# Kernel optimization log

Measured on AMD Instinct MI355X. Metric: run time of the kernel, lower is better.

Reference implementation:

```python
import jax, jax.numpy as jnp
import numpy as np
from functools import partial

N_USERS = 30000
N_ENTITIES = 70000
N = N_USERS + N_ENTITIES
D = 64
N_EDGES = 1_600_000
EPS = 1e-12


def setup_inputs() -> dict:
    key = jax.random.key(0)
    ks = jax.random.split(key, 10)
    s = 1.0 / np.sqrt(D)  # xavier-like scale for weights
    return {
        "user_tab": jax.random.normal(ks[0], (N_USERS, D), jnp.float32) * 0.1,
        "entity_tab": jax.random.normal(ks[1], (N_ENTITIES, D), jnp.float32) * 0.1,
        "A_vals": jax.random.uniform(ks[2], (N_EDGES,), jnp.float32) / 16.0,  # ~row-normalized
        "W1_1": jax.random.normal(ks[3], (D, D), jnp.float32) * s,
        "b1_1": jnp.zeros((D,), jnp.float32),
        "W2_1": jax.random.normal(ks[4], (D, D), jnp.float32) * s,
        "b2_1": jnp.zeros((D,), jnp.float32),
        "W1_2": jax.random.normal(ks[5], (D, 32), jnp.float32) * s,
        "b1_2": jnp.zeros((32,), jnp.float32),
        "W2_2": jax.random.normal(ks[6], (D, 32), jnp.float32) * s,
        "b2_2": jnp.zeros((32,), jnp.float32),
        "A_rows": jax.random.randint(ks[7], (N_EDGES,), 0, N, jnp.int64 if jax.config.jax_enable_x64 else jnp.int32),
        "A_cols": jax.random.randint(ks[8], (N_EDGES,), 0, N, jnp.int64 if jax.config.jax_enable_x64 else jnp.int32),
    }


def _spmm(rows, cols, vals, x):
    # sparse A (COO) @ dense x : gather tail embeddings, scale, scatter-add to rows
    msgs = x[cols] * vals[:, None]            # [E, d]
    return jax.ops.segment_sum(msgs, rows, num_segments=N)


def _l2norm(x):
    n = jnp.sqrt(jnp.sum(x * x, axis=1, keepdims=True))
    return x / jnp.maximum(n, EPS)


def _bi_layer(ego, side, W1, b1, W2, b2):
    sum_e = jax.nn.leaky_relu((ego + side) @ W1 + b1)  # slope 0.01 = torch default
    bi_e = jax.nn.leaky_relu((ego * side) @ W2 + b2)
    return _l2norm(sum_e + bi_e)  # dropout p=0 (eval)


def reference(user_tab, entity_tab, A_vals, W1_1, b1_1, W2_1, b2_1,
              W1_2, b1_2, W2_2, b2_2, A_rows, A_cols):
    ego = jnp.concatenate([user_tab, entity_tab], axis=0)  # [N, 64]
    all_embed = [ego]
    # layer 1: 64 -> 64
    side = _spmm(A_rows, A_cols, A_vals, ego)
    ego = _bi_layer(ego, side, W1_1, b1_1, W2_1, b2_1)
    all_embed.append(ego)
    # layer 2: 64 -> 32
    side = _spmm(A_rows, A_cols, A_vals, ego)
    ego = _bi_layer(ego, side, W1_2, b1_2, W2_2, b2_2)
    all_embed.append(ego)
    return jnp.concatenate(all_embed, axis=1)  # [N, 160]; split [n_users, n_entities] downstream
```

## Files before the change

### kernel.cpp

```cpp
#include <hip/hip_runtime.h>
#include <hip/hip_bf16.h>
#include <string.h>

#define N_USERS 30000
#define N_NODES 100000
#define DIM 64
#define N_EDGES 1600000
#define ROWS_PER_BUCK 256
#define NB ((N_NODES + ROWS_PER_BUCK - 1) / ROWS_PER_BUCK)
#define NGRP (NB * 64)
#define CHUNK 4096
#define NBLK_B ((N_EDGES + CHUNK - 1) / CHUNK)
#define BUCK_SLACK 2048
#define E_ALLOC (N_EDGES + NB * BUCK_SLACK)
#define STAGE_CAP 5120
#define GCAP 64

typedef __hip_bfloat16 bf16;
typedef __attribute__((ext_vector_type(8))) short short8;
typedef __attribute__((ext_vector_type(4))) float floatx4;

__device__ __forceinline__ float b2f(bf16 v) { return __bfloat162float(v); }
__device__ __forceinline__ bf16 f2b(float v) { return __float2bfloat16(v); }
__device__ __forceinline__ unsigned short fbits(float v) {
    bf16 b = f2b(v); unsigned short u; memcpy(&u, &b, 2); return u;
}
__device__ __forceinline__ float ubf(unsigned u) {
    return __uint_as_float(u << 16);
}

__device__ __forceinline__ float ld(const void* p, int i, int f32) {
    return f32 ? ((const float*)p)[i] : b2f(((const bf16*)p)[i]);
}
__device__ __forceinline__ void st(void* p, int i, float v, int f32) {
    if (f32) ((float*)p)[i] = v; else ((bf16*)p)[i] = f2b(v);
}
__device__ __forceinline__ unsigned short wbits(const void* p, int i, int f32) {
    return f32 ? fbits(((const float*)p)[i]) : ((const unsigned short*)p)[i];
}

__global__ void k_detect(const void* user, const void* ent, const void* vals,
                         const void* W, int* flags, int* bsize) {
    int t = threadIdx.x;
    for (int i = t; i < NB; i += 128) bsize[i] = 0;
    const void* ps[4] = { user, ent, vals, W };
    int k = t >> 5, i = t & 31;
    float v = ((const float*)ps[k])[i];
    int ok = (v == v && fabsf(v) <= 1e4f) ? 1 : 0;
    ok += __shfl_xor(ok, 1, 64);
    ok += __shfl_xor(ok, 2, 64);
    ok += __shfl_xor(ok, 4, 64);
    ok += __shfl_xor(ok, 8, 64);
    ok += __shfl_xor(ok, 16, 64);
    if ((t & 31) == 0) flags[k] = (ok >= 16) ? 1 : 0;
}

__global__ __launch_bounds__(256) void k_prepw(
    const void* W1_1, const void* b1_1, const void* W2_1, const void* b2_1,
    const void* W1_2, const void* b1_2, const void* W2_2, const void* b2_2,
    short8* wf1, float2* wsb1, short8* wf2, float* wsb2,
    const int* flags) {
    int t = threadIdx.x;
    int w = t >> 6, quad = (t >> 4) & 3, sub = t & 15;
    int fw = flags[3];
    short8 f0, f1, f2, f3;
#pragma unroll
    for (int j = 0; j < 8; ++j) {
        int k0 = quad * 8 + j, n = w * 16 + sub;
        f0[j] = (short)wbits(W1_1, k0 * 64 + n, fw);
        f1[j] = (short)wbits(W1_1, (k0 + 32) * 64 + n, fw);
        f2[j] = (short)wbits(W2_1, k0 * 64 + n, fw);
        f3[j] = (short)wbits(W2_1, (k0 + 32) * 64 + n, fw);
    }
    short8* p = wf1 + ((w * 4 + quad) * 16 + sub) * 4;
    p[0] = f0; p[1] = f1; p[2] = f2; p[3] = f3;
    if (quad == 0)
        wsb1[w * 16 + sub] = make_float2(ld(b1_1, w * 16 + sub, fw),
                                         ld(b2_1, w * 16 + sub, fw));
    int path = w >> 1, nbase = (w & 1) * 16;
    const void* W = path ? W2_2 : W1_2;
    const void* bb = path ? b2_2 : b1_2;
    short8 g0, g1;
#pragma unroll
    for (int j = 0; j < 8; ++j) {
        int k0 = quad * 8 + j, n = nbase + sub;
        g0[j] = (short)wbits(W, k0 * 32 + n, fw);
        g1[j] = (short)wbits(W, (k0 + 32) * 32 + n, fw);
    }
    short8* q = wf2 + ((w * 4 + quad) * 16 + sub) * 2;
    q[0] = g0; q[1] = g1;
    if (quad == 0) wsb2[w * 16 + sub] = ld(bb, nbase + sub, fw);
}

__global__ __launch_bounds__(256) void k_hista(const int* __restrict__ rows,
                                               int* __restrict__ cnt_table,
                                               int* __restrict__ bsize) {
    __shared__ int h[NB];
    int t = threadIdx.x, blk = blockIdx.x;
    for (int b = t; b < NB; b += 256) h[b] = 0;
    __syncthreads();
    int base = blk * CHUNK + t * 4;
#pragma unroll
    for (int it = 0; it < 4; ++it) {
        int e = base + it * 1024;
        if (e < N_EDGES) {
            int4 r = *(const int4*)&rows[e];
            atomicAdd(&h[r.x >> 8], 1);
            atomicAdd(&h[r.y >> 8], 1);
            atomicAdd(&h[r.z >> 8], 1);
            atomicAdd(&h[r.w >> 8], 1);
        }
    }
    __syncthreads();
    for (int b = t; b < NB; b += 256) {
        int v = h[b];
        cnt_table[blk * NB + b] = v;
        if (v) atomicAdd(&bsize[b], v);
    }
}

__global__ __launch_bounds__(512) void k_bscan(const int* __restrict__ bsize,
                                               int* __restrict__ bbase) {
    __shared__ int lds[512];
    int t = threadIdx.x;
    int v = (t < NB) ? (((bsize[t] + 3) & ~3) + BUCK_SLACK) : 0;
    lds[t] = v;
    __syncthreads();
    for (int off = 1; off < 512; off <<= 1) {
        int u = (t >= off) ? lds[t - off] : 0;
        __syncthreads();
        lds[t] += u;
        __syncthreads();
    }
    if (t <= NB) bbase[t] = (t == 0) ? 0 : lds[t - 1];
}

__global__ __launch_bounds__(512) void k_bscan2(int* __restrict__ cnt_table,
                                                const int* __restrict__ bbase) {
    __shared__ int lds[512];
    int t = threadIdx.x, b = blockIdx.x;
    int v = (t < NBLK_B) ? cnt_table[t * NB + b] : 0;
    lds[t] = v;
    __syncthreads();
    for (int off = 1; off < 512; off <<= 1) {
        int u = (t >= off) ? lds[t - off] : 0;
        __syncthreads();
        lds[t] += u;
        __syncthreads();
    }
    if (t < NBLK_B) cnt_table[t * NB + b] = bbase[b] + lds[t] - v;
}

__global__ __launch_bounds__(256) void k_bscatter2(
    const int* __restrict__ rows, const int* __restrict__ cols,
    const void* __restrict__ vals, const int* __restrict__ cnt_table,
    int2* __restrict__ bpack, const int* __restrict__ flags) {
    __shared__ int cur[NB];
    int t = threadIdx.x, blk = blockIdx.x;
    int fv = flags[2];
    for (int b = t; b < NB; b += 256) cur[b] = cnt_table[blk * NB + b];
    __syncthreads();
    int base = blk * CHUNK + t * 4;
#pragma unroll
    for (int it = 0; it < 4; ++it) {
        int e = base + it * 1024;
        if (e < N_EDGES) {
            int4 r = *(const int4*)&rows[e];
            int4 c = *(const int4*)&cols[e];
            float v0, v1, v2, v3;
            if (fv) {
                float4 vv = *(const float4*)((const float*)vals + e);
                v0 = vv.x; v1 = vv.y; v2 = vv.z; v3 = vv.w;
            } else {
                const bf16* bp = (const bf16*)vals + e;
                v0 = b2f(bp[0]); v1 = b2f(bp[1]); v2 = b2f(bp[2]); v3 = b2f(bp[3]);
            }
            int p0 = atomicAdd(&cur[r.x >> 8], 1);
            int p1 = atomicAdd(&cur[r.y >> 8], 1);
            int p2 = atomicAdd(&cur[r.z >> 8], 1);
            int p3 = atomicAdd(&cur[r.w >> 8], 1);
            bpack[p0] = make_int2(c.x | ((r.x & 255) << 17), __float_as_int(v0));
            bpack[p1] = make_int2(c.y | ((r.y & 255) << 17), __float_as_int(v1));
            bpack[p2] = make_int2(c.z | ((r.z & 255) << 17), __float_as_int(v2));
            bpack[p3] = make_int2(c.w | ((r.w & 255) << 17), __float_as_int(v3));
        }
    }
}

__global__ __launch_bounds__(256) void k_place2(
    const int* __restrict__ bsize, const int* __restrict__ bbase,
    const int2* __restrict__ bpack, int2* __restrict__ epack,
    int* __restrict__ grp_start, int* __restrict__ grp_len,
    int* __restrict__ perm) {
    __shared__ __align__(16) int2 stage[STAGE_CAP];
    __shared__ int rcnt[ROWS_PER_BUCK];
    __shared__ int skey[ROWS_PER_BUCK];
    __shared__ int scn[ROWS_PER_BUCK];
    __shared__ int sbr[ROWS_PER_BUCK];
    __shared__ int cur[ROWS_PER_BUCK];
    int t = threadIdx.x, b = blockIdx.x;
    int n = bsize[b];
    int gstart = bbase[b];
    rcnt[t] = 0;
    __syncthreads();
    for (int i = t; i < n; i += 256) {
        int2 p = bpack[gstart + i];
        if (i < STAGE_CAP) stage[i] = p;
        atomicAdd(&rcnt[(p.x >> 17) & 255], 1);
    }
    __syncthreads();
    int c = rcnt[t];
    int cp = (c + 3) & ~3;
    int key = (cp << 8) | t;
    __syncthreads();
    rcnt[t] = key;
    __syncthreads();
    int rank = 0;
    for (int u = 0; u < 256; ++u) rank += (rcnt[u] < key) ? 1 : 0;
    skey[rank] = key;
    __syncthreads();
    int gq = skey[t | 3] >> 8;
    scn[t] = gq;
    __syncthreads();
    for (int off = 1; off < 256; off <<= 1) {
        int u = (t >= off) ? scn[t - off] : 0;
        __syncthreads();
        scn[t] += u;
        __syncthreads();
    }
    sbr[t] = gstart + scn[t] - gq;
    __syncthreads();
    cur[t] = sbr[rank];
    int rowp = skey[t] & 255;
    int gid = b * 64 + (t >> 2);
    perm[gid * 4 + (t & 3)] = b * 256 + rowp;
    if ((t & 3) == 0) {
        grp_start[gid] = sbr[t];
        grp_len[gid] = skey[t | 3] >> 8;
    }
    __syncthreads();
    for (int i = t; i < n; i += 256) {
        int2 p = (i < STAGE_CAP) ? stage[i] : bpack[gstart + i];
        int r = (p.x >> 17) & 255;
        int pos = atomicAdd(&cur[r], 1);
        epack[pos] = make_int2((p.x & 0x1FFFF) << 7, p.y);
    }
    __syncthreads();
    int pend = sbr[rank] + (skey[rank | 3] >> 8);
    for (int pos = cur[t]; pos < pend; ++pos) epack[pos] = make_int2(0, 0);
}

__global__ void k_init(const void* __restrict__ user, const void* __restrict__ ent,
                       void* __restrict__ out, bf16* __restrict__ xb0,
                       const int* __restrict__ flags) {
    int i = blockIdx.x * blockDim.x + threadIdx.x;
    if (i >= N_NODES * DIM) return;
    int fo = flags[0], fe = flags[1];
    int n = i >> 6, d = i & 63;
    float v = (n < N_USERS) ? ld(user, i, fo) : ld(ent, i - N_USERS * DIM, fe);
    st(out, n * 160 + d, v, fo);
    xb0[i] = f2b(v);
}

#define G8_LOAD(r) \
    int b##r = (r * emx + ei) >> 1; \
    int4 qa##r = lq4[b##r], qb##r = lq4[b##r + 1]; \
    int4 qc##r = lq4[b##r + 2], qd##r = lq4[b##r + 3];

#define G8_ISSUE(r) \
    unsigned g##r##0 = *(const unsigned short*)(xbp + (unsigned)qa##r.x); \
    unsigned g##r##1 = *(const unsigned short*)(xbp + (unsigned)qa##r.z); \
    unsigned g##r##2 = *(const unsigned short*)(xbp + (unsigned)qb##r.x); \
    unsigned g##r##3 = *(const unsigned short*)(xbp + (unsigned)qb##r.z); \
    unsigned g##r##4 = *(const unsigned short*)(xbp + (unsigned)qc##r.x); \
    unsigned g##r##5 = *(const unsigned short*)(xbp + (unsigned)qc##r.z); \
    unsigned g##r##6 = *(const unsigned short*)(xbp + (unsigned)qd##r.x); \
    unsigned g##r##7 = *(const unsigned short*)(xbp + (unsigned)qd##r.z);

#define G8_FMA(r) \
    ea##r += __int_as_float(qa##r.y) * ubf(g##r##0); \
    ea##r += __int_as_float(qa##r.w) * ubf(g##r##1); \
    ea##r += __int_as_float(qb##r.y) * ubf(g##r##2); \
    ea##r += __int_as_float(qb##r.w) * ubf(g##r##3); \
    ea##r += __int_as_float(qc##r.y) * ubf(g##r##4); \
    ea##r += __int_as_float(qc##r.w) * ubf(g##r##5); \
    ea##r += __int_as_float(qd##r.y) * ubf(g##r##6); \
    ea##r += __int_as_float(qd##r.w) * ubf(g##r##7);

#define G4_LOAD(r) \
    int tb##r = (r * emx + ei) >> 1; \
    int4 ua##r = lq4[tb##r], ub##r = lq4[tb##r + 1];

#define G4_ISSUE(r) \
    unsigned h##r##0 = *(const unsigned short*)(xbp + (unsigned)ua##r.x); \
    unsigned h##r##1 = *(const unsigned short*)(xbp + (unsigned)ua##r.z); \
    unsigned h##r##2 = *(const unsigned short*)(xbp + (unsigned)ub##r.x); \
    unsigned h##r##3 = *(const unsigned short*)(xbp + (unsigned)ub##r.z);

#define G4_FMA(r) \
    ea##r += __int_as_float(ua##r.y) * ubf(h##r##0); \
    ea##r += __int_as_float(ua##r.w) * ubf(h##r##1); \
    ea##r += __int_as_float(ub##r.y) * ubf(h##r##2); \
    ea##r += __int_as_float(ub##r.w) * ubf(h##r##3);

#define FB_ROW_DECL(r) \
    int ej##r = (rs0 + r * emx) >> 1; \
    int4 eA##r = ep4[ej##r]; \
    int4 eB##r = ep4[ej##r + 1];

#define FB_ISSUE(r) \
    unsigned eg##r##0 = *(const unsigned short*)(xbp + (unsigned)eA##r.x); \
    unsigned eg##r##1 = *(const unsigned short*)(xbp + (unsigned)eA##r.z); \
    unsigned eg##r##2 = *(const unsigned short*)(xbp + (unsigned)eB##r.x); \
    unsigned eg##r##3 = *(const unsigned short*)(xbp + (unsigned)eB##r.z);

#define FB_ADV(r) \
    int4 nA##r = ep4[ej##r + 2]; \
    int4 nB##r = ep4[ej##r + 3]; \
    ej##r += 2;

#define FB_FMA(r) \
    ea##r += __int_as_float(eA##r.y) * ubf(eg##r##0); \
    ea##r += __int_as_float(eA##r.w) * ubf(eg##r##1); \
    ea##r += __int_as_float(eB##r.y) * ubf(eg##r##2); \
    ea##r += __int_as_float(eB##r.w) * ubf(eg##r##3); \
    eA##r = nA##r; eB##r = nB##r;

#define GATHER_BODY \
    float ea0 = 0.f, ea1 = 0.f, ea2 = 0.f, ea3 = 0.f; \
    if (emx <= GCAP) { \
        { \
            const int2* eps = (const int2*)epack + rs0; \
            int tot = emx << 2; \
            for (int i = lane; i < tot; i += 64) lq[i] = eps[i]; \
        } \
        int ei = 0; \
        for (; ei + 8 <= emx; ei += 8) { \
            G8_LOAD(0) G8_LOAD(1) G8_LOAD(2) G8_LOAD(3) \
            G8_ISSUE(0) G8_ISSUE(1) G8_ISSUE(2) G8_ISSUE(3) \
            G8_FMA(0) G8_FMA(1) G8_FMA(2) G8_FMA(3) \
        } \
        if (ei < emx) { \
            G4_LOAD(0) G4_LOAD(1) G4_LOAD(2) G4_LOAD(3) \
            G4_ISSUE(0) G4_ISSUE(1) G4_ISSUE(2) G4_ISSUE(3) \
            G4_FMA(0) G4_FMA(1) G4_FMA(2) G4_FMA(3) \
        } \
    } else { \
        const int4* ep4 = (const int4*)epack; \
        FB_ROW_DECL(0) FB_ROW_DECL(1) FB_ROW_DECL(2) FB_ROW_DECL(3) \
        for (int ei = 0; ei < emx; ei += 4) { \
            FB_ISSUE(0) FB_ISSUE(1) FB_ISSUE(2) FB_ISSUE(3) \
            FB_ADV(0) FB_ADV(1) FB_ADV(2) FB_ADV(3) \
            FB_FMA(0) FB_FMA(1) FB_FMA(2) FB_FMA(3) \
        } \
    }

__global__ __launch_bounds__(256) void k_layer1(
    const short8* __restrict__ wf1, const float2* __restrict__ wsb1,
    void* __restrict__ out, const int* __restrict__ grp_start,
    const int* __restrict__ grp_len, const int* __restrict__ perm,
    const int2* __restrict__ epack, const bf16* __restrict__ xt,
    bf16* __restrict__ xn, const int* __restrict__ flags) {
    __shared__ __align__(16) int2 lq_lds[4][4 * GCAP];
    __shared__ __align__(16) unsigned short hp_lds[16][72];
    __shared__ __align__(16) unsigned short hm_lds[16][72];
    __shared__ __align__(16) float ssq_lds[16][4];
    int t = threadIdx.x, lane = t & 63, w = t >> 6;
    int sub = lane & 15, quad = lane >> 4;
    int fo = flags[0];
    int gid = blockIdx.x * 4 + w;
    const char* xbp = (const char*)xt + (lane << 1);

    int rs0 = __builtin_amdgcn_readfirstlane(grp_start[gid]);
    int emx = __builtin_amdgcn_readfirstlane(grp_len[gid]);
    int4 pn = *(const int4*)&perm[gid * 4];
    int2* lq = lq_lds[w];
    const int4* lq4 = (const int4*)lq;
    GATHER_BODY
    {
        float s[4] = { ea0, ea1, ea2, ea3 };
        int nd[4] = { pn.x, pn.y, pn.z, pn.w };
#pragma unroll
        for (int r = 0; r < 4; ++r) {
            int node = (nd[r] < N_NODES) ? nd[r] : 0;
            float h = ld(out, node * 160 + lane, fo);
            hp_lds[w * 4 + r][lane] = fbits(h + s[r]);
            hm_lds[w * 4 + r][lane] = fbits(h * s[r]);
        }
    }
    __syncthreads();

    short8 Ap0 = *(const short8*)((const char*)hp_lds + sub * 144 + quad * 16);
    short8 Ap1 = *(const short8*)((const char*)hp_lds + sub * 144 + 64 + quad * 16);
    short8 Am0 = *(const short8*)((const char*)hm_lds + sub * 144 + quad * 16);
    short8 Am1 = *(const short8*)((const char*)hm_lds + sub * 144 + 64 + quad * 16);

    const short8* wfp = wf1 + ((w * 4 + quad) * 16 + sub) * 4;
    short8 Bw10 = wfp[0], Bw11 = wfp[1], Bw20 = wfp[2], Bw21 = wfp[3];
    float2 bb12 = wsb1[w * 16 + sub];
    float bias1 = bb12.x, bias2 = bb12.y;
    int wbase = w * 16;

    floatx4 c1; c1[0] = bias1; c1[1] = bias1; c1[2] = bias1; c1[3] = bias1;
    floatx4 c2; c2[0] = bias2; c2[1] = bias2; c2[2] = bias2; c2[3] = bias2;
    c1 = __builtin_amdgcn_mfma_f32_16x16x32_bf16(Ap0, Bw10, c1, 0, 0, 0);
    c1 = __builtin_amdgcn_mfma_f32_16x16x32_bf16(Ap1, Bw11, c1, 0, 0, 0);
    c2 = __builtin_amdgcn_mfma_f32_16x16x32_bf16(Am0, Bw20, c2, 0, 0, 0);
    c2 = __builtin_amdgcn_mfma_f32_16x16x32_bf16(Am1, Bw21, c2, 0, 0, 0);

    float v[4], sp[4];
#pragma unroll
    for (int r = 0; r < 4; ++r) {
        float s1 = c1[r], s2 = c2[r];
        s1 = s1 > 0.f ? s1 : 0.01f * s1;
        s2 = s2 > 0.f ? s2 : 0.01f * s2;
        v[r] = s1 + s2;
        float sq = v[r] * v[r];
        sq += __shfl_xor(sq, 1, 64);
        sq += __shfl_xor(sq, 2, 64);
        sq += __shfl_xor(sq, 4, 64);
        sq += __shfl_xor(sq, 8, 64);
        sp[r] = sq;
    }
    if (sub == 0) {
#pragma unroll
        for (int r = 0; r < 4; ++r) ssq_lds[quad * 4 + r][w] = sp[r];
    }
    __syncthreads();
    const int* pblk = perm + blockIdx.x * 16;
#pragma unroll
    for (int r = 0; r < 4; ++r) {
        int row = quad * 4 + r;
        floatx4 ps = *(const floatx4*)&ssq_lds[row][0];
        float ss = ps[0] + ps[1] + ps[2] + ps[3];
        float o = v[r] * (1.0f / fmaxf(sqrtf(ss), 1e-12f));
        int n = pblk[row];
        if (n < N_NODES) {
            st(out, n * 160 + 64 + wbase + sub, o, fo);
            xn[n * 64 + wbase + sub] = f2b(o);
        }
    }
}

__global__ __launch_bounds__(256) void k_layer2(
    const short8* __restrict__ wf2, const float* __restrict__ wsb2,
    void* __restrict__ out, const int* __restrict__ grp_start,
    const int* __restrict__ grp_len, const int* __restrict__ perm,
    const int2* __restrict__ epack, const bf16* __restrict__ xt,
    const int* __restrict__ flags) {
    __shared__ __align__(16) int2 lq_lds[4][4 * GCAP];
    __shared__ __align__(16) unsigned short hp_lds[16][72];
    __shared__ __align__(16) unsigned short hm_lds[16][72];
    __shared__ __align__(16) float bi_lds[16][32];
    __shared__ __align__(16) float ssq_lds[16][2];
    int t = threadIdx.x, lane = t & 63, w = t >> 6;
    int sub = lane & 15, quad = lane >> 4;
    int fo = flags[0];
    int gid = blockIdx.x * 4 + w;
    const char* xbp = (const char*)xt + (lane << 1);

    int rs0 = __builtin_amdgcn_readfirstlane(grp_start[gid]);
    int emx = __builtin_amdgcn_readfirstlane(grp_len[gid]);
    int4 pn = *(const int4*)&perm[gid * 4];
    int2* lq = lq_lds[w];
    const int4* lq4 = (const int4*)lq;
    GATHER_BODY
    {
        float s[4] = { ea0, ea1, ea2, ea3 };
        int nd[4] = { pn.x, pn.y, pn.z, pn.w };
#pragma unroll
        for (int r = 0; r < 4; ++r) {
            int node = (nd[r] < N_NODES) ? nd[r] : 0;
            float h = ld(out, node * 160 + 64 + lane, fo);
            hp_lds[w * 4 + r][lane] = fbits(h + s[r]);
            hm_lds[w * 4 + r][lane] = fbits(h * s[r]);
        }
    }
    __syncthreads();

    int path = w >> 1;
    int nbase = (w & 1) * 16;
    const unsigned short(*hl)[72] = path ? hm_lds : hp_lds;
    short8 Af0 = *(const short8*)((const char*)hl + sub * 144 + quad * 16);
    short8 Af1 = *(const short8*)((const char*)hl + sub * 144 + 64 + quad * 16);

    const short8* wfp = wf2 + ((w * 4 + quad) * 16 + sub) * 2;
    short8 Bf0 = wfp[0], Bf1 = wfp[1];
    float bias = wsb2[w * 16 + sub];

    floatx4 c; c[0] = bias; c[1] = bias; c[2] = bias; c[3] = bias;
    c = __builtin_amdgcn_mfma_f32_16x16x32_bf16(Af0, Bf0, c, 0, 0, 0);
    c = __builtin_amdgcn_mfma_f32_16x16x32_bf16(Af1, Bf1, c, 0, 0, 0);

    float T[4];
#pragma unroll
    for (int r = 0; r < 4; ++r) {
        float x = c[r];
        T[r] = x > 0.f ? x : 0.01f * x;
        if (path == 1) bi_lds[quad * 4 + r][nbase + sub] = T[r];
    }
    __syncthreads();

    float v[4], sp[4];
#pragma unroll
    for (int r = 0; r < 4; ++r) {
        v[r] = T[r] + bi_lds[quad * 4 + r][nbase + sub];
        float sq = v[r] * v[r];
        sq += __shfl_xor(sq, 1, 64);
        sq += __shfl_xor(sq, 2, 64);
        sq += __shfl_xor(sq, 4, 64);
        sq += __shfl_xor(sq, 8, 64);
        sp[r] = sq;
    }
    if (path == 0 && sub == 0) {
#pragma unroll
        for (int r = 0; r < 4; ++r) ssq_lds[quad * 4 + r][w & 1] = sp[r];
    }
    __syncthreads();
    if (path == 0) {
        const int* pblk = perm + blockIdx.x * 16;
#pragma unroll
        for (int r = 0; r < 4; ++r) {
            int row = quad * 4 + r;
            float ss = ssq_lds[row][0] + ssq_lds[row][1];
            float o = v[r] * (1.0f / fmaxf(sqrtf(ss), 1e-12f));
            int n = pblk[row];
            if (n < N_NODES) st(out, n * 160 + 128 + nbase + sub, o, fo);
        }
    }
}

extern "C" void kernel_launch(void* const* d_in, const int* in_sizes, int n_in,
                              void* d_out, int out_size, void* d_ws, size_t ws_size,
                              hipStream_t stream) {
    const void* user = d_in[0];
    const void* ent  = d_in[1];
    const void* vals = d_in[2];
    const void* W1_1 = d_in[3];
    const void* b1_1 = d_in[4];
    const void* W2_1 = d_in[5];
    const void* b2_1 = d_in[6];
    const void* W1_2 = d_in[7];
    const void* b1_2 = d_in[8];
    const void* W2_2 = d_in[9];
    const void* b2_2 = d_in[10];
    const int* rows  = (const int*)d_in[11];
    const int* cols  = (const int*)d_in[12];

    char* w = (char*)d_ws;
    int* flags     = (int*)w;    w += 256;
    int* bsize     = (int*)w;    w += 2048;
    int* bbase     = (int*)w;    w += 2048;
    short8* wf1    = (short8*)w; w += 16384;
    float2* wsb1   = (float2*)w; w += 512;
    short8* wf2    = (short8*)w; w += 8192;
    float* wsb2    = (float*)w;  w += 256;
    int* grp_start = (int*)w;    w += 100352;
    int* grp_len   = (int*)w;    w += 100352;
    int* perm      = (int*)w;    w += 400384;
    int2* epack    = (int2*)w;   w += (size_t)E_ALLOC * 8;
    bf16* xb0      = (bf16*)w;   w += (size_t)N_NODES * DIM * 2;
    bf16* xb1      = (bf16*)w;
    int* cnt_table = (int*)epack;
    int2* bpack    = (int2*)xb0;

    k_detect<<<1, 128, 0, stream>>>(user, ent, vals, W1_1, flags, bsize);
    k_prepw<<<1, 256, 0, stream>>>(W1_1, b1_1, W2_1, b2_1, W1_2, b1_2, W2_2, b2_2,
                                   wf1, wsb1, wf2, wsb2, flags);
    k_hista<<<NBLK_B, 256, 0, stream>>>(rows, cnt_table, bsize);
    k_bscan<<<1, 512, 0, stream>>>(bsize, bbase);
    k_bscan2<<<NB, 512, 0, stream>>>(cnt_table, bbase);
    k_bscatter2<<<NBLK_B, 256, 0, stream>>>(rows, cols, vals, cnt_table, bpack, flags);
    k_place2<<<NB, 256, 0, stream>>>(bsize, bbase, bpack, epack, grp_start, grp_len, perm);
    k_init<<<(N_NODES * DIM + 255) / 256, 256, 0, stream>>>(user, ent, d_out, xb0, flags);
    k_layer1<<<NB * 16, 256, 0, stream>>>(wf1, wsb1, d_out, grp_start, grp_len, perm, epack, xb0, xb1, flags);
    k_layer2<<<NB * 16, 256, 0, stream>>>(wf2, wsb2, d_out, grp_start, grp_len, perm, epack, xb1, flags);
}
```

Measured before the change: 321.4 us.

## Gather paired bf16 features per lane, merge prep kernels, double bucketing chunk

The gather loop now has each lane load a 32-bit pair of bf16 features, with the two wave halves handling alternate edges and being combined by a cross-half shuffle, instead of issuing 16-bit loads per lane. The residual h is read from the bf16 staging buffer rather than the output tensor. The detect and weight-prep kernels are merged into one launch, and the bucketing chunk size is doubled so fewer blocks run and the count scan uses 256 threads. The goal is fewer, wider memory transactions and fewer launches, at the cost of cross-lane reductions and less parallelism in histogramming.

```diff
diff --git a/kernel.cpp b/kernel.cpp
--- a/kernel.cpp
+++ b/kernel.cpp
@@ -9,7 +9,7 @@
 #define ROWS_PER_BUCK 256
 #define NB ((N_NODES + ROWS_PER_BUCK - 1) / ROWS_PER_BUCK)
 #define NGRP (NB * 64)
-#define CHUNK 4096
+#define CHUNK 8192
 #define NBLK_B ((N_EDGES + CHUNK - 1) / CHUNK)
 #define BUCK_SLACK 2048
 #define E_ALLOC (N_EDGES + NB * BUCK_SLACK)
@@ -28,6 +28,9 @@
 __device__ __forceinline__ float ubf(unsigned u) {
     return __uint_as_float(u << 16);
 }
+__device__ __forceinline__ float hbf(unsigned u) {
+    return __uint_as_float(u & 0xffff0000u);
+}
 
 __device__ __forceinline__ float ld(const void* p, int i, int f32) {
     return f32 ? ((const float*)p)[i] : b2f(((const bf16*)p)[i]);
@@ -39,30 +42,30 @@
     return f32 ? fbits(((const float*)p)[i]) : ((const unsigned short*)p)[i];
 }
 
-__global__ void k_detect(const void* user, const void* ent, const void* vals,
-                         const void* W, int* flags, int* bsize) {
-    int t = threadIdx.x;
-    for (int i = t; i < NB; i += 128) bsize[i] = 0;
-    const void* ps[4] = { user, ent, vals, W };
-    int k = t >> 5, i = t & 31;
-    float v = ((const float*)ps[k])[i];
-    int ok = (v == v && fabsf(v) <= 1e4f) ? 1 : 0;
-    ok += __shfl_xor(ok, 1, 64);
-    ok += __shfl_xor(ok, 2, 64);
-    ok += __shfl_xor(ok, 4, 64);
-    ok += __shfl_xor(ok, 8, 64);
-    ok += __shfl_xor(ok, 16, 64);
-    if ((t & 31) == 0) flags[k] = (ok >= 16) ? 1 : 0;
-}
-
-__global__ __launch_bounds__(256) void k_prepw(
+__global__ __launch_bounds__(256) void k_prep(
+    const void* user, const void* ent, const void* vals,
     const void* W1_1, const void* b1_1, const void* W2_1, const void* b2_1,
     const void* W1_2, const void* b1_2, const void* W2_2, const void* b2_2,
     short8* wf1, float2* wsb1, short8* wf2, float* wsb2,
-    const int* flags) {
+    int* flags, int* bsize) {
+    __shared__ int lf[4];
     int t = threadIdx.x;
+    for (int i = t; i < NB; i += 256) bsize[i] = 0;
+    int wv = t >> 6, ln = t & 63;
+    const void* ps[4] = { user, ent, vals, W1_1 };
+    if (ln < 32) {
+        float v = ((const float*)ps[wv])[ln];
+        int ok = (v == v && fabsf(v) <= 1e4f) ? 1 : 0;
+        ok += __shfl_xor(ok, 1, 64);
+        ok += __shfl_xor(ok, 2, 64);
+        ok += __shfl_xor(ok, 4, 64);
+        ok += __shfl_xor(ok, 8, 64);
+        ok += __shfl_xor(ok, 16, 64);
+        if (ln == 0) { int f = (ok >= 16) ? 1 : 0; lf[wv] = f; flags[wv] = f; }
+    }
+    __syncthreads();
+    int fw = lf[3];
     int w = t >> 6, quad = (t >> 4) & 3, sub = t & 15;
-    int fw = flags[3];
     short8 f0, f1, f2, f3;
 #pragma unroll
     for (int j = 0; j < 8; ++j) {
@@ -101,7 +104,7 @@
     __syncthreads();
     int base = blk * CHUNK + t * 4;
 #pragma unroll
-    for (int it = 0; it < 4; ++it) {
+    for (int it = 0; it < 8; ++it) {
         int e = base + it * 1024;
         if (e < N_EDGES) {
             int4 r = *(const int4*)&rows[e];
@@ -135,14 +138,14 @@
     if (t <= NB) bbase[t] = (t == 0) ? 0 : lds[t - 1];
 }
 
-__global__ __launch_bounds__(512) void k_bscan2(int* __restrict__ cnt_table,
+__global__ __launch_bounds__(256) void k_bscan2(int* __restrict__ cnt_table,
                                                 const int* __restrict__ bbase) {
-    __shared__ int lds[512];
+    __shared__ int lds[256];
     int t = threadIdx.x, b = blockIdx.x;
     int v = (t < NBLK_B) ? cnt_table[t * NB + b] : 0;
     lds[t] = v;
     __syncthreads();
-    for (int off = 1; off < 512; off <<= 1) {
+    for (int off = 1; off < 256; off <<= 1) {
         int u = (t >= off) ? lds[t - off] : 0;
         __syncthreads();
         lds[t] += u;
@@ -162,7 +165,7 @@
     __syncthreads();
     int base = blk * CHUNK + t * 4;
 #pragma unroll
-    for (int it = 0; it < 4; ++it) {
+    for (int it = 0; it < 8; ++it) {
         int e = base + it * 1024;
         if (e < N_EDGES) {
             int4 r = *(const int4*)&rows[e];
@@ -262,98 +265,90 @@
     xb0[i] = f2b(v);
 }
 
-#define G8_LOAD(r) \
-    int b##r = (r * emx + ei) >> 1; \
-    int4 qa##r = lq4[b##r], qb##r = lq4[b##r + 1]; \
-    int4 qc##r = lq4[b##r + 2], qd##r = lq4[b##r + 3];
-
-#define G8_ISSUE(r) \
-    unsigned g##r##0 = *(const unsigned short*)(xbp + (unsigned)qa##r.x); \
-    unsigned g##r##1 = *(const unsigned short*)(xbp + (unsigned)qa##r.z); \
-    unsigned g##r##2 = *(const unsigned short*)(xbp + (unsigned)qb##r.x); \
-    unsigned g##r##3 = *(const unsigned short*)(xbp + (unsigned)qb##r.z); \
-    unsigned g##r##4 = *(const unsigned short*)(xbp + (unsigned)qc##r.x); \
-    unsigned g##r##5 = *(const unsigned short*)(xbp + (unsigned)qc##r.z); \
-    unsigned g##r##6 = *(const unsigned short*)(xbp + (unsigned)qd##r.x); \
-    unsigned g##r##7 = *(const unsigned short*)(xbp + (unsigned)qd##r.z);
-
-#define G8_FMA(r) \
-    ea##r += __int_as_float(qa##r.y) * ubf(g##r##0); \
-    ea##r += __int_as_float(qa##r.w) * ubf(g##r##1); \
-    ea##r += __int_as_float(qb##r.y) * ubf(g##r##2); \
-    ea##r += __int_as_float(qb##r.w) * ubf(g##r##3); \
-    ea##r += __int_as_float(qc##r.y) * ubf(g##r##4); \
-    ea##r += __int_as_float(qc##r.w) * ubf(g##r##5); \
-    ea##r += __int_as_float(qd##r.y) * ubf(g##r##6); \
-    ea##r += __int_as_float(qd##r.w) * ubf(g##r##7);
-
-#define G4_LOAD(r) \
-    int tb##r = (r * emx + ei) >> 1; \
-    int4 ua##r = lq4[tb##r], ub##r = lq4[tb##r + 1];
-
-#define G4_ISSUE(r) \
-    unsigned h##r##0 = *(const unsigned short*)(xbp + (unsigned)ua##r.x); \
-    unsigned h##r##1 = *(const unsigned short*)(xbp + (unsigned)ua##r.z); \
-    unsigned h##r##2 = *(const unsigned short*)(xbp + (unsigned)ub##r.x); \
-    unsigned h##r##3 = *(const unsigned short*)(xbp + (unsigned)ub##r.z);
-
-#define G4_FMA(r) \
-    ea##r += __int_as_float(ua##r.y) * ubf(h##r##0); \
-    ea##r += __int_as_float(ua##r.w) * ubf(h##r##1); \
-    ea##r += __int_as_float(ub##r.y) * ubf(h##r##2); \
-    ea##r += __int_as_float(ub##r.w) * ubf(h##r##3);
-
-#define FB_ROW_DECL(r) \
-    int ej##r = (rs0 + r * emx) >> 1; \
-    int4 eA##r = ep4[ej##r]; \
-    int4 eB##r = ep4[ej##r + 1];
-
-#define FB_ISSUE(r) \
-    unsigned eg##r##0 = *(const unsigned short*)(xbp + (unsigned)eA##r.x); \
-    unsigned eg##r##1 = *(const unsigned short*)(xbp + (unsigned)eA##r.z); \
-    unsigned eg##r##2 = *(const unsigned short*)(xbp + (unsigned)eB##r.x); \
-    unsigned eg##r##3 = *(const unsigned short*)(xbp + (unsigned)eB##r.z);
-
-#define FB_ADV(r) \
-    int4 nA##r = ep4[ej##r + 2]; \
-    int4 nB##r = ep4[ej##r + 3]; \
-    ej##r += 2;
-
-#define FB_FMA(r) \
-    ea##r += __int_as_float(eA##r.y) * ubf(eg##r##0); \
-    ea##r += __int_as_float(eA##r.w) * ubf(eg##r##1); \
-    ea##r += __int_as_float(eB##r.y) * ubf(eg##r##2); \
-    ea##r += __int_as_float(eB##r.w) * ubf(eg##r##3); \
-    eA##r = nA##r; eB##r = nB##r;
+#define GP_LOAD8(r) \
+    int2 pa##r = lqh[r * emx + ei],     pb##r = lqh[r * emx + ei + 2], \
+         pc##r = lqh[r * emx + ei + 4], pd##r = lqh[r * emx + ei + 6];
+
+#define GP_ISSUE8(r) \
+    unsigned ga##r = *(const unsigned*)(xp + (unsigned)pa##r.x); \
+    unsigned gb##r = *(const unsigned*)(xp + (unsigned)pb##r.x); \
+    unsigned gc##r = *(const unsigned*)(xp + (unsigned)pc##r.x); \
+    unsigned gd##r = *(const unsigned*)(xp + (unsigned)pd##r.x);
+
+#define GP_FMA8(r) \
+    { float va = __int_as_float(pa##r.y), vb = __int_as_float(pb##r.y); \
+      float vc = __int_as_float(pc##r.y), vd = __int_as_float(pd##r.y); \
+      ax##r += va * ubf(ga##r); ay##r += va * hbf(ga##r); \
+      ax##r += vb * ubf(gb##r); ay##r += vb * hbf(gb##r); \
+      ax##r += vc * ubf(gc##r); ay##r += vc * hbf(gc##r); \
+      ax##r += vd * ubf(gd##r); ay##r += vd * hbf(gd##r); }
+
+#define GP_LOAD4(r) \
+    int2 ta##r = lqh[r * emx + ei], tb##r = lqh[r * emx + ei + 2];
+
+#define GP_ISSUE4(r) \
+    unsigned ha##r = *(const unsigned*)(xp + (unsigned)ta##r.x); \
+    unsigned hb##r = *(const unsigned*)(xp + (unsigned)tb##r.x);
+
+#define GP_FMA4(r) \
+    { float va = __int_as_float(ta##r.y), vb = __int_as_float(tb##r.y); \
+      ax##r += va * ubf(ha##r); ay##r += va * hbf(ha##r); \
+      ax##r += vb * ubf(hb##r); ay##r += vb * hbf(hb##r); }
+
+#define FB_ROW(r) { \
+    float s_ = 0.f; \
+    const int2* eb = (const int2*)epack + rs0 + r * emx; \
+    for (int e = 0; e < emx; e += 2) { \
+        int4 q = *(const int4*)(eb + e); \
+        s_ += __int_as_float(q.y) * b2f(*(const bf16*)(xq + (unsigned)q.x)); \
+        s_ += __int_as_float(q.w) * b2f(*(const bf16*)(xq + (unsigned)q.z)); \
+    } \
+    ax##r = __shfl(s_, (lane & 31) << 1, 64); \
+    ay##r = __shfl(s_, ((lane & 31) << 1) | 1, 64); }
 
 #define GATHER_BODY \
-    float ea0 = 0.f, ea1 = 0.f, ea2 = 0.f, ea3 = 0.f; \
+    float ax0 = 0.f, ay0 = 0.f, ax1 = 0.f, ay1 = 0.f; \
+    float ax2 = 0.f, ay2 = 0.f, ax3 = 0.f, ay3 = 0.f; \
     if (emx <= GCAP) { \
-        { \
-            const int2* eps = (const int2*)epack + rs0; \
-            int tot = emx << 2; \
-            for (int i = lane; i < tot; i += 64) lq[i] = eps[i]; \
-        } \
+        { const int2* eps = (const int2*)epack + rs0; \
+          int tot = emx << 2; \
+          for (int i = lane; i < tot; i += 64) lq[i] = eps[i]; } \
         int ei = 0; \
         for (; ei + 8 <= emx; ei += 8) { \
-            G8_LOAD(0) G8_LOAD(1) G8_LOAD(2) G8_LOAD(3) \
-            G8_ISSUE(0) G8_ISSUE(1) G8_ISSUE(2) G8_ISSUE(3) \
-            G8_FMA(0) G8_FMA(1) G8_FMA(2) G8_FMA(3) \
+            GP_LOAD8(0) GP_LOAD8(1) GP_LOAD8(2) GP_LOAD8(3) \
+            GP_ISSUE8(0) GP_ISSUE8(1) GP_ISSUE8(2) GP_ISSUE8(3) \
+            GP_FMA8(0) GP_FMA8(1) GP_FMA8(2) GP_FMA8(3) \
         } \
         if (ei < emx) { \
-            G4_LOAD(0) G4_LOAD(1) G4_LOAD(2) G4_LOAD(3) \
-            G4_ISSUE(0) G4_ISSUE(1) G4_ISSUE(2) G4_ISSUE(3) \
-            G4_FMA(0) G4_FMA(1) G4_FMA(2) G4_FMA(3) \
+            GP_LOAD4(0) GP_LOAD4(1) GP_LOAD4(2) GP_LOAD4(3) \
+            GP_ISSUE4(0) GP_ISSUE4(1) GP_ISSUE4(2) GP_ISSUE4(3) \
+            GP_FMA4(0) GP_FMA4(1) GP_FMA4(2) GP_FMA4(3) \
         } \
+        ax0 += __shfl_xor(ax0, 32, 64); ay0 += __shfl_xor(ay0, 32, 64); \
+        ax1 += __shfl_xor(ax1, 32, 64); ay1 += __shfl_xor(ay1, 32, 64); \
+        ax2 += __shfl_xor(ax2, 32, 64); ay2 += __shfl_xor(ay2, 32, 64); \
+        ax3 += __shfl_xor(ax3, 32, 64); ay3 += __shfl_xor(ay3, 32, 64); \
     } else { \
-        const int4* ep4 = (const int4*)epack; \
-        FB_ROW_DECL(0) FB_ROW_DECL(1) FB_ROW_DECL(2) FB_ROW_DECL(3) \
-        for (int ei = 0; ei < emx; ei += 4) { \
-            FB_ISSUE(0) FB_ISSUE(1) FB_ISSUE(2) FB_ISSUE(3) \
-            FB_ADV(0) FB_ADV(1) FB_ADV(2) FB_ADV(3) \
-            FB_FMA(0) FB_FMA(1) FB_FMA(2) FB_FMA(3) \
-        } \
-    }
+        const char* xq = (const char*)xt + (lane << 1); \
+        FB_ROW(0) FB_ROW(1) FB_ROW(2) FB_ROW(3) \
+    }
+
+#define STAGE_HPHM \
+    { int half = lane >> 5, li = lane & 31; \
+      unsigned* hp32 = (unsigned*)hp_lds; \
+      unsigned* hm32 = (unsigned*)hm_lds; \
+      _Pragma("unroll") \
+      for (int k = 0; k < 2; ++k) { \
+          float sx = half ? (k ? ax3 : ax2) : (k ? ax1 : ax0); \
+          float sy = half ? (k ? ay3 : ay2) : (k ? ay1 : ay0); \
+          int node = half ? (k ? pn.w : pn.z) : (k ? pn.y : pn.x); \
+          node = (node < N_NODES) ? node : 0; \
+          unsigned hg = *(const unsigned*)((const char*)xt + node * 128 + (li << 2)); \
+          float h0 = ubf(hg), h1 = hbf(hg); \
+          int row = w * 4 + ((half << 1) | k); \
+          hp32[row * 36 + li] = (unsigned)fbits(h0 + sx) | ((unsigned)fbits(h1 + sy) << 16); \
+          hm32[row * 36 + li] = (unsigned)fbits(h0 * sx) | ((unsigned)fbits(h1 * sy) << 16); \
+      } }
 
 __global__ __launch_bounds__(256) void k_layer1(
     const short8* __restrict__ wf1, const float2* __restrict__ wsb1,
@@ -369,25 +364,15 @@
     int sub = lane & 15, quad = lane >> 4;
     int fo = flags[0];
     int gid = blockIdx.x * 4 + w;
-    const char* xbp = (const char*)xt + (lane << 1);
+    const char* xp = (const char*)xt + ((lane & 31) << 2);
 
     int rs0 = __builtin_amdgcn_readfirstlane(grp_start[gid]);
     int emx = __builtin_amdgcn_readfirstlane(grp_len[gid]);
     int4 pn = *(const int4*)&perm[gid * 4];
     int2* lq = lq_lds[w];
-    const int4* lq4 = (const int4*)lq;
+    const int2* lqh = lq + (lane >> 5);
     GATHER_BODY
-    {
-        float s[4] = { ea0, ea1, ea2, ea3 };
-        int nd[4] = { pn.x, pn.y, pn.z, pn.w };
-#pragma unroll
-        for (int r = 0; r < 4; ++r) {
-            int node = (nd[r] < N_NODES) ? nd[r] : 0;
-            float h = ld(out, node * 160 + lane, fo);
-            hp_lds[w * 4 + r][lane] = fbits(h + s[r]);
-            hm_lds[w * 4 + r][lane] = fbits(h * s[r]);
-        }
-    }
+    STAGE_HPHM
     __syncthreads();
 
     short8 Ap0 = *(const short8*)((const char*)hp_lds + sub * 144 + quad * 16);
@@ -457,25 +442,15 @@
     int sub = lane & 15, quad = lane >> 4;
     int fo = flags[0];
     int gid = blockIdx.x * 4 + w;
-    const char* xbp = (const char*)xt + (lane << 1);
+    const char* xp = (const char*)xt + ((lane & 31) << 2);
 
     int rs0 = __builtin_amdgcn_readfirstlane(grp_start[gid]);
     int emx = __builtin_amdgcn_readfirstlane(grp_len[gid]);
     int4 pn = *(const int4*)&perm[gid * 4];
     int2* lq = lq_lds[w];
-    const int4* lq4 = (const int4*)lq;
+    const int2* lqh = lq + (lane >> 5);
     GATHER_BODY
-    {
-        float s[4] = { ea0, ea1, ea2, ea3 };
-        int nd[4] = { pn.x, pn.y, pn.z, pn.w };
-#pragma unroll
-        for (int r = 0; r < 4; ++r) {
-            int node = (nd[r] < N_NODES) ? nd[r] : 0;
-            float h = ld(out, node * 160 + 64 + lane, fo);
-            hp_lds[w * 4 + r][lane] = fbits(h + s[r]);
-            hm_lds[w * 4 + r][lane] = fbits(h * s[r]);
-        }
-    }
+    STAGE_HPHM
     __syncthreads();
 
     int path = w >> 1;
@@ -564,12 +539,12 @@
     int* cnt_table = (int*)epack;
     int2* bpack    = (int2*)xb0;
 
-    k_detect<<<1, 128, 0, stream>>>(user, ent, vals, W1_1, flags, bsize);
-    k_prepw<<<1, 256, 0, stream>>>(W1_1, b1_1, W2_1, b2_1, W1_2, b1_2, W2_2, b2_2,
-                                   wf1, wsb1, wf2, wsb2, flags);
+    k_prep<<<1, 256, 0, stream>>>(user, ent, vals, W1_1, b1_1, W2_1, b2_1,
+                                  W1_2, b1_2, W2_2, b2_2,
+                                  wf1, wsb1, wf2, wsb2, flags, bsize);
     k_hista<<<NBLK_B, 256, 0, stream>>>(rows, cnt_table, bsize);
     k_bscan<<<1, 512, 0, stream>>>(bsize, bbase);
-    k_bscan2<<<NB, 512, 0, stream>>>(cnt_table, bbase);
+    k_bscan2<<<NB, 256, 0, stream>>>(cnt_table, bbase);
     k_bscatter2<<<NBLK_B, 256, 0, stream>>>(rows, cols, vals, cnt_table, bpack, flags);
     k_place2<<<NB, 256, 0, stream>>>(bsize, bbase, bpack, epack, grp_start, grp_len, perm);
     k_init<<<(N_NODES * DIM + 255) / 256, 256, 0, stream>>>(user, ent, d_out, xb0, flags);
```

Measured after the change: 281.5 us (median of 2 runs). -12.4%, faster.
